# Optimization experiments

Measured on AMD Instinct MI355X. Metric: run time of the kernel, lower is better.

## Reference

```python
import jax, jax.numpy as jnp
import numpy as np

N = 262144
IN_DIM = 64
HID = 256
EMB = 128
OUT = 64
B = 16
MAX_AISLES = 64
NUM_SEG = B * MAX_AISLES  # static upper bound on number of (batch, aisle) segments


def setup_inputs() -> dict:
    key = jax.random.key(0)
    ks = jax.random.split(key, 16)
    def lin(k, fan_in, fan_out):
        bound = 1.0 / np.sqrt(fan_in)
        kw, kb = jax.random.split(k)
        W = jax.random.uniform(kw, (fan_in, fan_out), jnp.float32, -bound, bound)
        b = jax.random.uniform(kb, (fan_out,), jnp.float32, -bound, bound)
        return W, b
    W1, b1 = lin(ks[0], IN_DIM, HID)
    W2, b2 = lin(ks[1], HID, HID)
    W3, b3 = lin(ks[2], HID, EMB)
    A1, c1 = lin(ks[3], 2 * EMB, HID)
    A2, c2 = lin(ks[4], HID, HID)
    A3, c3 = lin(ks[5], HID, OUT)
    x = jax.random.normal(ks[6], (N, IN_DIM), jnp.float32)
    aisle_nrs = jax.random.randint(ks[7], (N,), 0, MAX_AISLES, jnp.int32)
    batch = jnp.sort(jax.random.randint(ks[8], (N,), 0, B, jnp.int32))
    return {"x": x, "aisle_nrs": aisle_nrs, "batch": batch,
            "W1": W1, "b1": b1, "W2": W2, "b2": b2, "W3": W3, "b3": b3,
            "A1": A1, "c1": c1, "A2": A2, "c2": c2, "A3": A3, "c3": c3}


def reference(x, aisle_nrs, batch, W1, b1, W2, b2, W3, b3, A1, c1, A2, c2, A3, c3):
    lrelu = lambda v: jax.nn.leaky_relu(v, 0.01)  # torch LeakyReLU default slope
    h = lrelu(x @ W1 + b1)
    h = lrelu(h @ W2 + b2)
    h = h @ W3 + b3  # [N, EMB]
    # dynamic group id: aisle + batch * (max_aisle + 1)
    aisle_ids = aisle_nrs + batch * (jnp.max(aisle_nrs) + 1)
    # scatter-mean over segments (NUM_SEG is a static upper bound)
    sums = jax.ops.segment_sum(h, aisle_ids, num_segments=NUM_SEG)
    counts = jax.ops.segment_sum(jnp.ones((h.shape[0],), h.dtype), aisle_ids,
                                 num_segments=NUM_SEG)
    means = sums / jnp.maximum(counts, 1.0)[:, None]
    # gather back and concat
    z = jnp.concatenate([h, means[aisle_ids]], axis=1)  # [N, 2*EMB]
    z = lrelu(z @ A1 + c1)
    z = lrelu(z @ A2 + c2)
    z = z @ A3 + c3
    return z
```

## Files before the change

### kernel.cpp

```cpp
#include <hip/hip_runtime.h>
#include <hip/hip_bf16.h>

#define N_ROWS 262144
#define IN_DIM 64
#define HID 256
#define EMB 128
#define OUT_DIM 64
#define NSEG 1024
#define ROWS_B 128
#define MT 8
#define NWAVE 8
#define LDS_S 264
#define CHUNK 1024
#define NSLOTS (2 * (N_ROWS / CHUNK))

typedef _Float16 h16;
typedef _Float16 h16x8 __attribute__((ext_vector_type(8)));
typedef _Float16 h16x4 __attribute__((ext_vector_type(4)));
typedef float f32x4 __attribute__((ext_vector_type(4)));


__global__ void k_max(const int* __restrict__ aisle, int* __restrict__ maxA) {
    int v = 0;
    for (int i = blockIdx.x * blockDim.x + threadIdx.x; i < N_ROWS; i += gridDim.x * blockDim.x)
        v = max(v, aisle[i]);
#pragma unroll
    for (int off = 32; off > 0; off >>= 1) v = max(v, __shfl_down(v, off));
    __shared__ int red[4];
    if ((threadIdx.x & 63) == 0) red[threadIdx.x >> 6] = v;
    __syncthreads();
    if (threadIdx.x == 0) {
        int m = red[0];
        for (int i = 1; i < 4; ++i) m = max(m, red[i]);
        atomicMax(maxA, m);
    }
}

__device__ __forceinline__ void frag_nk(int o, int K, int& n, int& k) {
    int tile = o / (16 * K);
    int r = o - tile * 16 * K;
    n = tile * 16 + ((r >> 3) & 15);
    k = (r >> 9) * 32 + (((r >> 7) & 3) << 3) + (r & 7);
}

__global__ void k_prep_weights(const float* __restrict__ W1, const float* __restrict__ W2,
                               const float* __restrict__ W3, const float* __restrict__ A1f,
                               const float* __restrict__ A2f, const float* __restrict__ A3f,
                               h16* __restrict__ W1t, h16* __restrict__ W2t, h16* __restrict__ W3t,
                               h16* __restrict__ A1t, h16* __restrict__ A2t, h16* __restrict__ A3t) {
    int idx = blockIdx.x * 256 + threadIdx.x;
    int n, k;
    if (idx < 16384)       { int o = idx;          frag_nk(o, 64, n, k);  W1t[o] = (h16)W1[k * 256 + n]; }
    else if (idx < 81920)  { int o = idx - 16384;  frag_nk(o, 256, n, k); W2t[o] = (h16)W2[k * 256 + n]; }
    else if (idx < 114688) { int o = idx - 81920;  frag_nk(o, 256, n, k); W3t[o] = (h16)W3[k * 128 + n]; }
    else if (idx < 180224) { int o = idx - 114688; frag_nk(o, 256, n, k); A1t[o] = (h16)A1f[k * 256 + n]; }
    else if (idx < 245760) { int o = idx - 180224; frag_nk(o, 256, n, k); A2t[o] = (h16)A2f[k * 256 + n]; }
    else                   { int o = idx - 245760; frag_nk(o, 256, n, k); A3t[o] = (h16)A3f[k * 64  + n]; }
}

template <int K, int NOUT, bool ACT>
__device__ __forceinline__ void mlp_layer_ip(const h16* __restrict__ Wt,
                                             const float* __restrict__ bias,
                                             h16* __restrict__ S,
                                             int lane, int wave) {
    constexpr int NW = NOUT / NWAVE;
    constexpr int NT = NW / 16;
    constexpr int KT = K / 32;
    const int l15 = lane & 15, l4 = lane >> 4;
    f32x4 acc[MT][NT];
#pragma unroll
    for (int mt = 0; mt < MT; ++mt)
#pragma unroll
        for (int nt = 0; nt < NT; ++nt)
#pragma unroll
            for (int j = 0; j < 4; ++j) acc[mt][nt][j] = 0.f;

    const h16* wb[NT];
#pragma unroll
    for (int nt = 0; nt < NT; ++nt)
        wb[nt] = Wt + (size_t)(wave * NT + nt) * 16 * K + lane * 8;

    h16x8 b0[NT], b1[NT];
#pragma unroll
    for (int nt = 0; nt < NT; ++nt) b0[nt] = *(const h16x8*)wb[nt];
    if (KT > 1) {
#pragma unroll
        for (int nt = 0; nt < NT; ++nt) b1[nt] = *(const h16x8*)(wb[nt] + 512);
    }

#pragma unroll
    for (int kt = 0; kt < KT; ++kt) {
        h16x8 bc[NT];
#pragma unroll
        for (int nt = 0; nt < NT; ++nt) bc[nt] = b0[nt];
#pragma unroll
        for (int nt = 0; nt < NT; ++nt) b0[nt] = b1[nt];
        if (kt + 2 < KT) {
#pragma unroll
            for (int nt = 0; nt < NT; ++nt) b1[nt] = *(const h16x8*)(wb[nt] + (kt + 2) * 512);
        }
#pragma unroll
        for (int mt = 0; mt < MT; ++mt) {
            h16x8 a = *(const h16x8*)&S[(mt * 16 + l15) * LDS_S + kt * 32 + l4 * 8];
#pragma unroll
            for (int nt = 0; nt < NT; ++nt)
                acc[mt][nt] = __builtin_amdgcn_mfma_f32_16x16x32_f16(bc[nt], a, acc[mt][nt], 0, 0, 0);
        }
    }

    __syncthreads();

#pragma unroll
    for (int nt = 0; nt < NT; ++nt) {
        const int cb = wave * NW + nt * 16 + l4 * 4;
        const f32x4 bias4 = *(const f32x4*)&bias[cb];
#pragma unroll
        for (int mt = 0; mt < MT; ++mt) {
            f32x4 v = acc[mt][nt] + bias4;
            if (ACT) {
#pragma unroll
                for (int j = 0; j < 4; ++j) v[j] = (v[j] > 0.f) ? v[j] : 0.01f * v[j];
            }
            h16x4 hv;
#pragma unroll
            for (int j = 0; j < 4; ++j) hv[j] = (h16)v[j];
            *(h16x4*)&S[(mt * 16 + l15) * LDS_S + cb] = hv;
        }
    }
    __syncthreads();
}

__device__ __forceinline__ void mlp_layer_out_h16(const h16* __restrict__ Wt,
                                                  const float* __restrict__ bias,
                                                  const h16* __restrict__ S,
                                                  h16* __restrict__ gout, int row0,
                                                  int lane, int wave) {
    const int l15 = lane & 15, l4 = lane >> 4;
    f32x4 acc[MT];
#pragma unroll
    for (int mt = 0; mt < MT; ++mt)
#pragma unroll
        for (int j = 0; j < 4; ++j) acc[mt][j] = 0.f;

    const h16* wb = Wt + (size_t)wave * 16 * 256 + lane * 8;
    h16x8 b0 = *(const h16x8*)wb;
    h16x8 b1 = *(const h16x8*)(wb + 512);
#pragma unroll
    for (int kt = 0; kt < 8; ++kt) {
        h16x8 bc = b0;
        b0 = b1;
        if (kt + 2 < 8) b1 = *(const h16x8*)(wb + (kt + 2) * 512);
#pragma unroll
        for (int mt = 0; mt < MT; ++mt) {
            h16x8 a = *(const h16x8*)&S[(mt * 16 + l15) * LDS_S + kt * 32 + l4 * 8];
            acc[mt] = __builtin_amdgcn_mfma_f32_16x16x32_f16(bc, a, acc[mt], 0, 0, 0);
        }
    }

    const int cb = wave * 16 + l4 * 4;
    const f32x4 bias4 = *(const f32x4*)&bias[cb];
#pragma unroll
    for (int mt = 0; mt < MT; ++mt) {
        f32x4 v = acc[mt] + bias4;
        h16x4 hv;
#pragma unroll
        for (int j = 0; j < 4; ++j) hv[j] = (h16)v[j];
        *(h16x4*)&gout[(size_t)(row0 + mt * 16 + l15) * 128 + cb] = hv;
    }
}

__global__ __launch_bounds__(512, 4) void k1(const float* __restrict__ x,
                                             const h16* __restrict__ W1t, const float* __restrict__ b1,
                                             const h16* __restrict__ W2t, const float* __restrict__ b2,
                                             const h16* __restrict__ W3t, const float* __restrict__ b3,
                                             h16* __restrict__ hbuf) {
    __shared__ __align__(16) h16 S[ROWS_B * LDS_S];
    const int tid = threadIdx.x, lane = tid & 63, wave = tid >> 6;
    const int row0 = blockIdx.x * ROWS_B;

    {
        const int r = tid >> 2, c16 = (tid & 3) * 16;
        const float* src = &x[(size_t)(row0 + r) * 64 + c16];
        f32x4 v0 = *(const f32x4*)&src[0];
        f32x4 v1 = *(const f32x4*)&src[4];
        f32x4 v2 = *(const f32x4*)&src[8];
        f32x4 v3 = *(const f32x4*)&src[12];
        h16x8 h0, h1;
#pragma unroll
        for (int j = 0; j < 4; ++j) { h0[j] = (h16)v0[j]; h0[4 + j] = (h16)v1[j];
                                      h1[j] = (h16)v2[j]; h1[4 + j] = (h16)v3[j]; }
        *(h16x8*)&S[r * LDS_S + c16]     = h0;
        *(h16x8*)&S[r * LDS_S + c16 + 8] = h1;
    }
    __syncthreads();

    mlp_layer_ip<64, 256, true>(W1t, b1, S, lane, wave);
    mlp_layer_ip<256, 256, true>(W2t, b2, S, lane, wave);
    mlp_layer_out_h16(W3t, b3, S, hbuf, row0, lane, wave);
}

__global__ __launch_bounds__(256) void k_scatter(const h16* __restrict__ hbuf,
                                                 const int* __restrict__ aisle,
                                                 const int* __restrict__ batch,
                                                 float* __restrict__ partials,
                                                 float* __restrict__ pcount,
                                                 int* __restrict__ bvmap) {
    __shared__ int la[CHUNK], lb[CHUNK], rankv[CHUNK], rowlist[CHUNK];
    __shared__ int hist[128], scan[128];
    const int tid = threadIdx.x;
    const int row0 = blockIdx.x * CHUNK;

    if (tid < 128) hist[tid] = 0;
    for (int i = tid; i < CHUNK; i += 256) { la[i] = aisle[row0 + i]; lb[i] = batch[row0 + i]; }
    __syncthreads();

    const int bLo = lb[0], bHi = lb[CHUNK - 1];

    for (int i = tid; i < CHUNK; i += 256) {
        int slot = min(lb[i] - bLo, 1);
        rankv[i] = atomicAdd(&hist[slot * 64 + la[i]], 1);
    }
    __syncthreads();
    if (tid < 128) scan[tid] = hist[tid];
    __syncthreads();
#pragma unroll
    for (int st = 1; st < 128; st <<= 1) {
        int v = 0;
        if (tid < 128 && tid >= st) v = scan[tid - st];
        __syncthreads();
        if (tid < 128) scan[tid] += v;
        __syncthreads();
    }
    for (int i = tid; i < CHUNK; i += 256) {
        int bin = min(lb[i] - bLo, 1) * 64 + la[i];
        rowlist[scan[bin] - hist[bin] + rankv[i]] = i;
    }
    __syncthreads();

    const int a_own = tid >> 2, cg = tid & 3;
    for (int slot = 0; slot < 2; ++slot) {
        const int sid = blockIdx.x * 2 + slot;
        const int bv = bLo + slot;
        if (bv > bHi) { if (tid == 0) bvmap[sid] = -1; continue; }

        const int bin = slot * 64 + a_own;
        const int s1 = scan[bin];
        const int s0 = s1 - hist[bin];

        float acc[32];
#pragma unroll
        for (int j = 0; j < 32; ++j) acc[j] = 0.f;

        for (int idx = s0; idx < s1; ++idx) {
            const int r = rowlist[idx];
            const h16x8* src = (const h16x8*)&hbuf[(size_t)(row0 + r) * 128 + cg * 32];
            h16x8 v0 = src[0], v1 = src[1], v2 = src[2], v3 = src[3];
#pragma unroll
            for (int j = 0; j < 8; ++j) {
                acc[j]      += (float)v0[j];
                acc[8 + j]  += (float)v1[j];
                acc[16 + j] += (float)v2[j];
                acc[24 + j] += (float)v3[j];
            }
        }
        float* dst = &partials[(size_t)sid * 8192 + tid * 32];
#pragma unroll
        for (int g2 = 0; g2 < 8; ++g2) *(f32x4*)&dst[g2 * 4] = *(const f32x4*)&acc[g2 * 4];
        if (cg == 0) pcount[sid * 64 + a_own] = (float)(s1 - s0);
        if (tid == 0) bvmap[sid] = bv;
    }
}

__global__ __launch_bounds__(128) void k_means(const float* __restrict__ partials,
                                               const float* __restrict__ pcount,
                                               const int* __restrict__ bvmap,
                                               h16* __restrict__ means,
                                               const int* __restrict__ maxA) {
    __shared__ int sbv[NSLOTS];
    const int b = blockIdx.x >> 6, a = blockIdx.x & 63;
    const int tid = threadIdx.x;
    const int mult = *maxA + 1;
    for (int i = tid; i < NSLOTS; i += 128) sbv[i] = bvmap[i];
    __syncthreads();
    if (a >= mult) return;

    float sum = 0.f, cnt = 0.f;
    for (int s = 0; s < NSLOTS; ++s) {
        if (sbv[s] == b) {
            sum += partials[(size_t)s * 8192 + a * 128 + tid];
            cnt += pcount[s * 64 + a];
        }
    }
    means[(size_t)(b * mult + a) * 128 + tid] = (h16)(sum / fmaxf(cnt, 1.0f));
}

__global__ __launch_bounds__(512, 4) void k3(const h16* __restrict__ hbuf,
                                             const int* __restrict__ aisle,
                                             const int* __restrict__ batch,
                                             const h16* __restrict__ means,
                                             const h16* __restrict__ A1t, const float* __restrict__ c1,
                                             const h16* __restrict__ A2t, const float* __restrict__ c2,
                                             const h16* __restrict__ A3t, const float* __restrict__ c3,
                                             float* __restrict__ out, const int* __restrict__ maxA) {
    __shared__ __align__(16) h16 S[ROWS_B * LDS_S];
    const int tid = threadIdx.x, lane = tid & 63, wave = tid >> 6;
    const int row0 = blockIdx.x * ROWS_B;
    const int mult = *maxA + 1;

    {
        const int r = tid >> 2, p = tid & 3;
        const int g = row0 + r;
        const h16x8* hs = (const h16x8*)&hbuf[(size_t)g * 128 + p * 32];
        h16x8* hd = (h16x8*)&S[r * LDS_S + p * 32];
        hd[0] = hs[0]; hd[1] = hs[1]; hd[2] = hs[2]; hd[3] = hs[3];
        const int id = aisle[g] + batch[g] * mult;
        const h16x8* ms = (const h16x8*)&means[(size_t)id * 128 + p * 32];
        h16x8* md = (h16x8*)&S[r * LDS_S + 128 + p * 32];
        md[0] = ms[0]; md[1] = ms[1]; md[2] = ms[2]; md[3] = ms[3];
    }
    __syncthreads();

    mlp_layer_ip<256, 256, true>(A1t, c1, S, lane, wave);
    mlp_layer_ip<256, 256, true>(A2t, c2, S, lane, wave);

    {
        const int l15 = lane & 15, l4 = lane >> 4;
        const int w4 = wave & 3, kw = wave >> 2;
        f32x4 acc4[MT];
#pragma unroll
        for (int mt = 0; mt < MT; ++mt)
#pragma unroll
            for (int j = 0; j < 4; ++j) acc4[mt][j] = 0.f;

        const h16* wb = A3t + (size_t)w4 * 16 * 256 + (size_t)kw * 4 * 512 + lane * 8;
        h16x8 b0 = *(const h16x8*)wb;
        h16x8 b1 = *(const h16x8*)(wb + 512);
#pragma unroll
        for (int kt = 0; kt < 4; ++kt) {
            h16x8 bc = b0;
            b0 = b1;
            if (kt + 2 < 4) b1 = *(const h16x8*)(wb + (kt + 2) * 512);
#pragma unroll
            for (int mt = 0; mt < MT; ++mt) {
                h16x8 a = *(const h16x8*)&S[(mt * 16 + l15) * LDS_S + kw * 128 + kt * 32 + l4 * 8];
                acc4[mt] = __builtin_amdgcn_mfma_f32_16x16x32_f16(bc, a, acc4[mt], 0, 0, 0);
            }
        }
        __syncthreads();
        float* fS = (float*)S;
        if (kw == 1) {
#pragma unroll
            for (int mt = 0; mt < MT; ++mt) {
                const int row = mt * 16 + l15;
                *(f32x4*)&fS[row * 68 + w4 * 16 + l4 * 4] = acc4[mt];
            }
        }
        __syncthreads();
        if (kw == 0) {
            const f32x4 bias4 = *(const f32x4*)&c3[w4 * 16 + l4 * 4];
#pragma unroll
            for (int mt = 0; mt < MT; ++mt) {
                const int row = mt * 16 + l15;
                f32x4 p = *(const f32x4*)&fS[row * 68 + w4 * 16 + l4 * 4];
                f32x4 v = acc4[mt] + p + bias4;
                *(f32x4*)&out[(size_t)(row0 + row) * 64 + w4 * 16 + l4 * 4] = v;
            }
        }
    }
}

extern "C" void kernel_launch(void* const* d_in, const int* in_sizes, int n_in,
                              void* d_out, int out_size, void* d_ws, size_t ws_size,
                              hipStream_t stream) {
    const float* x     = (const float*)d_in[0];
    const int*   aisle = (const int*)d_in[1];
    const int*   batch = (const int*)d_in[2];
    const float* W1 = (const float*)d_in[3];  const float* b1 = (const float*)d_in[4];
    const float* W2 = (const float*)d_in[5];  const float* b2 = (const float*)d_in[6];
    const float* W3 = (const float*)d_in[7];  const float* b3 = (const float*)d_in[8];
    const float* A1 = (const float*)d_in[9];  const float* c1 = (const float*)d_in[10];
    const float* A2 = (const float*)d_in[11]; const float* c2 = (const float*)d_in[12];
    const float* A3 = (const float*)d_in[13]; const float* c3 = (const float*)d_in[14];
    float* out = (float*)d_out;

    char* w = (char*)d_ws;
    size_t off = 0;
    h16*   hbuf     = (h16*)(w + off);   off += (size_t)N_ROWS * 128 * sizeof(h16);
    float* partials = (float*)(w + off); off += (size_t)NSLOTS * 8192 * sizeof(float);
    float* pcount   = (float*)(w + off); off += NSLOTS * 64 * sizeof(float);
    int*   bvmap    = (int*)(w + off);   off += NSLOTS * sizeof(int);
    h16*   means    = (h16*)(w + off);   off += NSEG * 128 * sizeof(h16);
    h16*   W1t      = (h16*)(w + off);   off += 16384 * sizeof(h16);
    h16*   W2t      = (h16*)(w + off);   off += 65536 * sizeof(h16);
    h16*   W3t      = (h16*)(w + off);   off += 32768 * sizeof(h16);
    h16*   A1t      = (h16*)(w + off);   off += 65536 * sizeof(h16);
    h16*   A2t      = (h16*)(w + off);   off += 65536 * sizeof(h16);
    h16*   A3t      = (h16*)(w + off);   off += 16384 * sizeof(h16);
    int*   maxA     = (int*)(w + off);   off += 256;

    hipMemsetAsync(maxA, 0, sizeof(int), stream);

    k_max<<<256, 256, 0, stream>>>(aisle, maxA);
    k_prep_weights<<<1024, 256, 0, stream>>>(W1, W2, W3, A1, A2, A3, W1t, W2t, W3t, A1t, A2t, A3t);
    k1<<<N_ROWS / ROWS_B, 512, 0, stream>>>(x, W1t, b1, W2t, b2, W3t, b3, hbuf);
    k_scatter<<<N_ROWS / CHUNK, 256, 0, stream>>>(hbuf, aisle, batch, partials, pcount, bvmap);
    k_means<<<16 * 64, 128, 0, stream>>>(partials, pcount, bvmap, means, maxA);
    k3<<<N_ROWS / ROWS_B, 512, 0, stream>>>(hbuf, aisle, batch, means, A1t, c1, A2t, c2, A3t, c3,
                                            out, maxA);
}
```

Measured before the change: 381.2 us.

## Use 2x4 wave tiling with XOR-swizzled unpadded LDS rows in MLP layers

Reorganizes the per-block MLP GEMMs so the 8 waves form a 2x4 grid, each computing a 64-row by 64-column tile instead of all 128 rows by 32 columns. Each wave now reuses each A fragment across 4 weight fragments and loads half as many LDS A fragments. The padded LDS row stride of 264 is replaced by an unpadded 256 stride with an XOR swizzle on 16-byte chunks, which keeps ds_read conflicts low and shrinks LDS use. Weight prefetch depth drops from two k-steps to one, which may expose more global load latency.

```diff
diff --git a/kernel.cpp b/kernel.cpp
--- a/kernel.cpp
+++ b/kernel.cpp
@@ -8,9 +8,8 @@
 #define OUT_DIM 64
 #define NSEG 1024
 #define ROWS_B 128
-#define MT 8
 #define NWAVE 8
-#define LDS_S 264
+#define SROW 256
 #define CHUNK 1024
 #define NSLOTS (2 * (N_ROWS / CHUNK))
 
@@ -18,6 +17,7 @@
 typedef _Float16 h16x8 __attribute__((ext_vector_type(8)));
 typedef _Float16 h16x4 __attribute__((ext_vector_type(4)));
 typedef float f32x4 __attribute__((ext_vector_type(4)));
+
 
 
 __global__ void k_max(const int* __restrict__ aisle, int* __restrict__ maxA) {
@@ -58,52 +58,47 @@
     else                   { int o = idx - 245760; frag_nk(o, 256, n, k); A3t[o] = (h16)A3f[k * 64  + n]; }
 }
 
-template <int K, int NOUT, bool ACT>
+template <int K, bool ACT>
 __device__ __forceinline__ void mlp_layer_ip(const h16* __restrict__ Wt,
                                              const float* __restrict__ bias,
                                              h16* __restrict__ S,
                                              int lane, int wave) {
-    constexpr int NW = NOUT / NWAVE;
-    constexpr int NT = NW / 16;
     constexpr int KT = K / 32;
     const int l15 = lane & 15, l4 = lane >> 4;
-    f32x4 acc[MT][NT];
-#pragma unroll
-    for (int mt = 0; mt < MT; ++mt)
-#pragma unroll
-        for (int nt = 0; nt < NT; ++nt)
+    const int wr = wave >> 2, wc = wave & 3;
+    const int sw = (l15 & 7) << 2;
+    f32x4 acc[4][4];
+#pragma unroll
+    for (int mt = 0; mt < 4; ++mt)
+#pragma unroll
+        for (int nt = 0; nt < 4; ++nt)
 #pragma unroll
             for (int j = 0; j < 4; ++j) acc[mt][nt][j] = 0.f;
 
-    const h16* wb[NT];
-#pragma unroll
-    for (int nt = 0; nt < NT; ++nt)
-        wb[nt] = Wt + (size_t)(wave * NT + nt) * 16 * K + lane * 8;
-
-    h16x8 b0[NT], b1[NT];
-#pragma unroll
-    for (int nt = 0; nt < NT; ++nt) b0[nt] = *(const h16x8*)wb[nt];
-    if (KT > 1) {
-#pragma unroll
-        for (int nt = 0; nt < NT; ++nt) b1[nt] = *(const h16x8*)(wb[nt] + 512);
-    }
+    const h16* wb[4];
+#pragma unroll
+    for (int nt = 0; nt < 4; ++nt)
+        wb[nt] = Wt + (size_t)(wc * 4 + nt) * 16 * K + lane * 8;
+
+    h16x8 bn[4];
+#pragma unroll
+    for (int nt = 0; nt < 4; ++nt) bn[nt] = *(const h16x8*)wb[nt];
 
 #pragma unroll
     for (int kt = 0; kt < KT; ++kt) {
-        h16x8 bc[NT];
-#pragma unroll
-        for (int nt = 0; nt < NT; ++nt) bc[nt] = b0[nt];
-#pragma unroll
-        for (int nt = 0; nt < NT; ++nt) b0[nt] = b1[nt];
-        if (kt + 2 < KT) {
-#pragma unroll
-            for (int nt = 0; nt < NT; ++nt) b1[nt] = *(const h16x8*)(wb[nt] + (kt + 2) * 512);
-        }
-#pragma unroll
-        for (int mt = 0; mt < MT; ++mt) {
-            h16x8 a = *(const h16x8*)&S[(mt * 16 + l15) * LDS_S + kt * 32 + l4 * 8];
-#pragma unroll
-            for (int nt = 0; nt < NT; ++nt)
+        h16x8 bc[4];
+#pragma unroll
+        for (int nt = 0; nt < 4; ++nt) bc[nt] = bn[nt];
+        if (kt + 1 < KT) {
+#pragma unroll
+            for (int nt = 0; nt < 4; ++nt) bn[nt] = *(const h16x8*)(wb[nt] + (kt + 1) * 512);
+        }
+#pragma unroll
+        for (int mt = 0; mt < 4; ++mt) {
+            const int row = wr * 64 + mt * 16 + l15;
+            h16x8 a = *(const h16x8*)&S[row * SROW + (((kt * 4 + l4) ^ sw) << 3)];
+#pragma unroll
+            for (int nt = 0; nt < 4; ++nt)
                 acc[mt][nt] = __builtin_amdgcn_mfma_f32_16x16x32_f16(bc[nt], a, acc[mt][nt], 0, 0, 0);
         }
     }
@@ -111,11 +106,13 @@
     __syncthreads();
 
 #pragma unroll
-    for (int nt = 0; nt < NT; ++nt) {
-        const int cb = wave * NW + nt * 16 + l4 * 4;
+    for (int nt = 0; nt < 4; ++nt) {
+        const int cb = wc * 64 + nt * 16 + l4 * 4;
         const f32x4 bias4 = *(const f32x4*)&bias[cb];
-#pragma unroll
-        for (int mt = 0; mt < MT; ++mt) {
+        const int ch = cb >> 3, co = cb & 7;
+#pragma unroll
+        for (int mt = 0; mt < 4; ++mt) {
+            const int row = wr * 64 + mt * 16 + l15;
             f32x4 v = acc[mt][nt] + bias4;
             if (ACT) {
 #pragma unroll
@@ -124,7 +121,7 @@
             h16x4 hv;
 #pragma unroll
             for (int j = 0; j < 4; ++j) hv[j] = (h16)v[j];
-            *(h16x4*)&S[(mt * 16 + l15) * LDS_S + cb] = hv;
+            *(h16x4*)&S[row * SROW + ((ch ^ sw) << 3) + co] = hv;
         }
     }
     __syncthreads();
@@ -136,36 +133,57 @@
                                                   h16* __restrict__ gout, int row0,
                                                   int lane, int wave) {
     const int l15 = lane & 15, l4 = lane >> 4;
-    f32x4 acc[MT];
-#pragma unroll
-    for (int mt = 0; mt < MT; ++mt)
-#pragma unroll
-        for (int j = 0; j < 4; ++j) acc[mt][j] = 0.f;
-
-    const h16* wb = Wt + (size_t)wave * 16 * 256 + lane * 8;
-    h16x8 b0 = *(const h16x8*)wb;
-    h16x8 b1 = *(const h16x8*)(wb + 512);
+    const int wr = wave >> 2, wc = wave & 3;
+    const int sw = (l15 & 7) << 2;
+    f32x4 acc[4][2];
+#pragma unroll
+    for (int mt = 0; mt < 4; ++mt)
+#pragma unroll
+        for (int nt = 0; nt < 2; ++nt)
+#pragma unroll
+            for (int j = 0; j < 4; ++j) acc[mt][nt][j] = 0.f;
+
+    const h16* wb[2];
+#pragma unroll
+    for (int nt = 0; nt < 2; ++nt)
+        wb[nt] = Wt + (size_t)(wc * 2 + nt) * 16 * 256 + lane * 8;
+
+    h16x8 bn[2];
+#pragma unroll
+    for (int nt = 0; nt < 2; ++nt) bn[nt] = *(const h16x8*)wb[nt];
+
 #pragma unroll
     for (int kt = 0; kt < 8; ++kt) {
-        h16x8 bc = b0;
-        b0 = b1;
-        if (kt + 2 < 8) b1 = *(const h16x8*)(wb + (kt + 2) * 512);
-#pragma unroll
-        for (int mt = 0; mt < MT; ++mt) {
-            h16x8 a = *(const h16x8*)&S[(mt * 16 + l15) * LDS_S + kt * 32 + l4 * 8];
-            acc[mt] = __builtin_amdgcn_mfma_f32_16x16x32_f16(bc, a, acc[mt], 0, 0, 0);
-        }
-    }
-
-    const int cb = wave * 16 + l4 * 4;
-    const f32x4 bias4 = *(const f32x4*)&bias[cb];
-#pragma unroll
-    for (int mt = 0; mt < MT; ++mt) {
-        f32x4 v = acc[mt] + bias4;
-        h16x4 hv;
-#pragma unroll
-        for (int j = 0; j < 4; ++j) hv[j] = (h16)v[j];
-        *(h16x4*)&gout[(size_t)(row0 + mt * 16 + l15) * 128 + cb] = hv;
+        h16x8 bc[2];
+#pragma unroll
+        for (int nt = 0; nt < 2; ++nt) bc[nt] = bn[nt];
+        if (kt + 1 < 8) {
+#pragma unroll
+            for (int nt = 0; nt < 2; ++nt) bn[nt] = *(const h16x8*)(wb[nt] + (kt + 1) * 512);
+        }
+#pragma unroll
+        for (int mt = 0; mt < 4; ++mt) {
+            const int row = wr * 64 + mt * 16 + l15;
+            h16x8 a = *(const h16x8*)&S[row * SROW + (((kt * 4 + l4) ^ sw) << 3)];
+#pragma unroll
+            for (int nt = 0; nt < 2; ++nt)
+                acc[mt][nt] = __builtin_amdgcn_mfma_f32_16x16x32_f16(bc[nt], a, acc[mt][nt], 0, 0, 0);
+        }
+    }
+
+#pragma unroll
+    for (int nt = 0; nt < 2; ++nt) {
+        const int cb = wc * 32 + nt * 16 + l4 * 4;
+        const f32x4 bias4 = *(const f32x4*)&bias[cb];
+#pragma unroll
+        for (int mt = 0; mt < 4; ++mt) {
+            const int row = wr * 64 + mt * 16 + l15;
+            f32x4 v = acc[mt][nt] + bias4;
+            h16x4 hv;
+#pragma unroll
+            for (int j = 0; j < 4; ++j) hv[j] = (h16)v[j];
+            *(h16x4*)&gout[(size_t)(row0 + row) * 128 + cb] = hv;
+        }
     }
 }
 
@@ -174,28 +192,29 @@
                                              const h16* __restrict__ W2t, const float* __restrict__ b2,
                                              const h16* __restrict__ W3t, const float* __restrict__ b3,
                                              h16* __restrict__ hbuf) {
-    __shared__ __align__(16) h16 S[ROWS_B * LDS_S];
+    __shared__ __align__(16) h16 S[ROWS_B * SROW];
     const int tid = threadIdx.x, lane = tid & 63, wave = tid >> 6;
     const int row0 = blockIdx.x * ROWS_B;
 
     {
-        const int r = tid >> 2, c16 = (tid & 3) * 16;
-        const float* src = &x[(size_t)(row0 + r) * 64 + c16];
-        f32x4 v0 = *(const f32x4*)&src[0];
-        f32x4 v1 = *(const f32x4*)&src[4];
-        f32x4 v2 = *(const f32x4*)&src[8];
-        f32x4 v3 = *(const f32x4*)&src[12];
-        h16x8 h0, h1;
-#pragma unroll
-        for (int j = 0; j < 4; ++j) { h0[j] = (h16)v0[j]; h0[4 + j] = (h16)v1[j];
-                                      h1[j] = (h16)v2[j]; h1[4 + j] = (h16)v3[j]; }
-        *(h16x8*)&S[r * LDS_S + c16]     = h0;
-        *(h16x8*)&S[r * LDS_S + c16 + 8] = h1;
-    }
-    __syncthreads();
-
-    mlp_layer_ip<64, 256, true>(W1t, b1, S, lane, wave);
-    mlp_layer_ip<256, 256, true>(W2t, b2, S, lane, wave);
+        const int r = tid >> 2, p = tid & 3;
+        const int sw = (r & 7) << 2;
+#pragma unroll
+        for (int i = 0; i < 2; ++i) {
+            const int c = p + i * 4;
+            const float* src = &x[(size_t)(row0 + r) * 64 + c * 8];
+            f32x4 v0 = *(const f32x4*)&src[0];
+            f32x4 v1 = *(const f32x4*)&src[4];
+            h16x8 hv;
+#pragma unroll
+            for (int j = 0; j < 4; ++j) { hv[j] = (h16)v0[j]; hv[4 + j] = (h16)v1[j]; }
+            *(h16x8*)&S[r * SROW + ((c ^ sw) << 3)] = hv;
+        }
+    }
+    __syncthreads();
+
+    mlp_layer_ip<64, true>(W1t, b1, S, lane, wave);
+    mlp_layer_ip<256, true>(W2t, b2, S, lane, wave);
     mlp_layer_out_h16(W3t, b3, S, hbuf, row0, lane, wave);
 }
 
@@ -302,7 +321,7 @@
                                              const h16* __restrict__ A2t, const float* __restrict__ c2,
                                              const h16* __restrict__ A3t, const float* __restrict__ c3,
                                              float* __restrict__ out, const int* __restrict__ maxA) {
-    __shared__ __align__(16) h16 S[ROWS_B * LDS_S];
+    __shared__ __align__(16) h16 S[ROWS_B * SROW];
     const int tid = threadIdx.x, lane = tid & 63, wave = tid >> 6;
     const int row0 = blockIdx.x * ROWS_B;
     const int mult = *maxA + 1;
@@ -310,39 +329,47 @@
     {
         const int r = tid >> 2, p = tid & 3;
         const int g = row0 + r;
-        const h16x8* hs = (const h16x8*)&hbuf[(size_t)g * 128 + p * 32];
-        h16x8* hd = (h16x8*)&S[r * LDS_S + p * 32];
-        hd[0] = hs[0]; hd[1] = hs[1]; hd[2] = hs[2]; hd[3] = hs[3];
+        const int sw = (r & 7) << 2;
         const int id = aisle[g] + batch[g] * mult;
-        const h16x8* ms = (const h16x8*)&means[(size_t)id * 128 + p * 32];
-        h16x8* md = (h16x8*)&S[r * LDS_S + 128 + p * 32];
-        md[0] = ms[0]; md[1] = ms[1]; md[2] = ms[2]; md[3] = ms[3];
-    }
-    __syncthreads();
-
-    mlp_layer_ip<256, 256, true>(A1t, c1, S, lane, wave);
-    mlp_layer_ip<256, 256, true>(A2t, c2, S, lane, wave);
+#pragma unroll
+        for (int i = 0; i < 4; ++i) {
+            const int c = p + i * 4;
+            *(h16x8*)&S[r * SROW + ((c ^ sw) << 3)] =
+                *(const h16x8*)&hbuf[(size_t)g * 128 + c * 8];
+        }
+#pragma unroll
+        for (int i = 0; i < 4; ++i) {
+            const int c = p + i * 4;
+            *(h16x8*)&S[r * SROW + (((16 + c) ^ sw) << 3)] =
+                *(const h16x8*)&means[(size_t)id * 128 + c * 8];
+        }
+    }
+    __syncthreads();
+
+    mlp_layer_ip<256, true>(A1t, c1, S, lane, wave);
+    mlp_layer_ip<256, true>(A2t, c2, S, lane, wave);
 
     {
         const int l15 = lane & 15, l4 = lane >> 4;
+        const int sw = (l15 & 7) << 2;
         const int w4 = wave & 3, kw = wave >> 2;
-        f32x4 acc4[MT];
-#pragma unroll
-        for (int mt = 0; mt < MT; ++mt)
+        f32x4 acc4[8];
+#pragma unroll
+        for (int mt = 0; mt < 8; ++mt)
 #pragma unroll
             for (int j = 0; j < 4; ++j) acc4[mt][j] = 0.f;
 
         const h16* wb = A3t + (size_t)w4 * 16 * 256 + (size_t)kw * 4 * 512 + lane * 8;
-        h16x8 b0 = *(const h16x8*)wb;
-        h16x8 b1 = *(const h16x8*)(wb + 512);
+        h16x8 bn = *(const h16x8*)wb;
 #pragma unroll
         for (int kt = 0; kt < 4; ++kt) {
-            h16x8 bc = b0;
-            b0 = b1;
-            if (kt + 2 < 4) b1 = *(const h16x8*)(wb + (kt + 2) * 512);
-#pragma unroll
-            for (int mt = 0; mt < MT; ++mt) {
-                h16x8 a = *(const h16x8*)&S[(mt * 16 + l15) * LDS_S + kw * 128 + kt * 32 + l4 * 8];
+            h16x8 bc = bn;
+            if (kt + 1 < 4) bn = *(const h16x8*)(wb + (kt + 1) * 512);
+#pragma unroll
+            for (int mt = 0; mt < 8; ++mt) {
+                const int row = mt * 16 + l15;
+                const int c = kw * 16 + kt * 4 + l4;
+                h16x8 a = *(const h16x8*)&S[row * SROW + ((c ^ sw) << 3)];
                 acc4[mt] = __builtin_amdgcn_mfma_f32_16x16x32_f16(bc, a, acc4[mt], 0, 0, 0);
             }
         }
@@ -350,7 +377,7 @@
         float* fS = (float*)S;
         if (kw == 1) {
 #pragma unroll
-            for (int mt = 0; mt < MT; ++mt) {
+            for (int mt = 0; mt < 8; ++mt) {
                 const int row = mt * 16 + l15;
                 *(f32x4*)&fS[row * 68 + w4 * 16 + l4 * 4] = acc4[mt];
             }
@@ -359,7 +386,7 @@
         if (kw == 0) {
             const f32x4 bias4 = *(const f32x4*)&c3[w4 * 16 + l4 * 4];
 #pragma unroll
-            for (int mt = 0; mt < MT; ++mt) {
+            for (int mt = 0; mt < 8; ++mt) {
                 const int row = mt * 16 + l15;
                 f32x4 p = *(const f32x4*)&fS[row * 68 + w4 * 16 + l4 * 4];
                 f32x4 v = acc4[mt] + p + bias4;
```

After: 391.5 us. +2.7%, slower.
